# Kernel tuning notes

Hardware: AMD Instinct MI355X
Metric: run time of the kernel (lower is better)

Reference implementation:

```python
import jax, jax.numpy as jnp
import numpy as np
from jax import lax

B, T, D, H = 128, 512, 512, 512
FORGET_BIAS = 1.0  # TF BasicLSTMCell default


def setup_inputs() -> dict:
    key = jax.random.key(0)
    k1, k2, k3 = jax.random.split(key, 3)
    scale = 1.0 / np.sqrt(D + H)
    return {
        "word_vectors": jax.random.normal(k1, (B, T, D), dtype=jnp.float32),
        "num_words": jax.random.randint(k2, (B,), 0, T, dtype=jnp.int32),
        "init_c": jnp.zeros((B, H), dtype=jnp.float32),
        "init_h": jnp.zeros((B, H), dtype=jnp.float32),
        "W": jax.random.normal(k3, (D + H, 4 * H), dtype=jnp.float32) * scale,  # gates i,j,f,o
        "b": jnp.zeros((4 * H,), dtype=jnp.float32),
    }


def reference(word_vectors, num_words, init_c, init_h, W, b):
    # word_vectors: [B, T, D] -> time-major [T, B, D]
    xs = jnp.transpose(word_vectors, (1, 0, 2))
    ts = jnp.arange(T, dtype=num_words.dtype)

    def step(carry, inp):
        c, h = carry
        x, t = inp
        z = jnp.concatenate([x, h], axis=-1) @ W + b  # [B, 4H]
        i, j, f, o = jnp.split(z, 4, axis=-1)  # TF gate order
        new_c = c * jax.nn.sigmoid(f + FORGET_BIAS) + jax.nn.sigmoid(i) * jnp.tanh(j)
        new_h = jnp.tanh(new_c) * jax.nn.sigmoid(o)
        mask = (t < num_words)[:, None]  # [B, 1]
        # static_rnn sequence_length semantics: copy state through, zero outputs
        c2 = jnp.where(mask, new_c, c)
        h2 = jnp.where(mask, new_h, h)
        out = jnp.where(mask, new_h, jnp.zeros_like(new_h))
        return (c2, h2), out

    (final_c, final_h), outputs = lax.scan(step, (init_c, init_h), (xs, ts))
    # outputs: [T, B, H] (time-major, like the list returned by static_rnn)
    return outputs, final_c, final_h
```

## Files before the change

### kernel.cpp

```cpp
#include <hip/hip_runtime.h>


#define B_ 128
#define T_ 512
#define D_ 512
#define H_ 512
#define POLL_CAP 8192

typedef __bf16 bf16x8 __attribute__((ext_vector_type(8)));
typedef float f32x4 __attribute__((ext_vector_type(4)));
typedef unsigned long long u64;

static __device__ __forceinline__ unsigned short f2bf(float f) {
  return __builtin_bit_cast(unsigned short, (__bf16)f);
}
static __device__ __forceinline__ float fast_sigmoid(float x) {
  return __builtin_amdgcn_rcpf(1.f + __expf(-x));
}
static __device__ __forceinline__ float fast_tanh(float x) {
  float xc = fminf(fmaxf(x, -15.f), 15.f);
  float t = __expf(-2.f * xc);
  return (1.f - t) * __builtin_amdgcn_rcpf(1.f + t);
}

#define LBAR()                                             \
  do {                                                     \
    __asm__ volatile("s_waitcnt lgkmcnt(0)" ::: "memory"); \
    __builtin_amdgcn_s_barrier();                          \
    __asm__ volatile("" ::: "memory");                     \
  } while (0)

__global__ __launch_bounds__(256) void pack_w_kernel(const float* __restrict__ W,
                                                     unsigned short* __restrict__ Wp) {
  int tid = blockIdx.x * 256 + threadIdx.x;
  int j = tid & 7;
  int lane = (tid >> 3) & 63;
  int f = tid >> 9;
  int kt = f & 31;
  int w = (f >> 5) & 7;
  int hb = f >> 8;
  int k = (kt << 5) + ((lane >> 4) << 3) + j;
  int cb = lane & 15;
  int col = ((cb >> 2) << 9) + (hb << 5) + (w << 2) + (cb & 3);
  Wp[tid] = f2bf(W[k * 2048 + col]);
}

__global__ __launch_bounds__(1024) void init_ws_kernel(unsigned int* __restrict__ hg) {
  hg[blockIdx.x * 1024 + threadIdx.x] = 0u;
}

__global__ __launch_bounds__(512, 2) void lstm_persistent(
    const float* __restrict__ wv, const int* __restrict__ nw,
    const float* __restrict__ ic, const float* __restrict__ ih,
    const float* __restrict__ bias, const unsigned short* __restrict__ Wp,
    unsigned int* __restrict__ hg, float* __restrict__ out) {
  __shared__ __align__(16) unsigned short hlds[2][16 * 512];
  __shared__ __align__(16) unsigned short xlds[2][16 * 512];

  const int tid = threadIdx.x;
  const int wgid = blockIdx.x;
  const int mg = wgid & 7;
  const int hb = wgid >> 3;
  const int w = tid >> 6;
  const int lane = tid & 63;

  const int q = lane >> 4;
  const int gp = (lane >> 2) & 3;
  const int hc = lane & 3;
  const int er = (q << 2) + gp;
  const int kin = (w << 2) | hc;
  const int grow = (mg << 4) + er;
  const int gcol = (hb << 5) + kin;

  const int nwv = nw[grow];
  float c_reg = ic[grow * H_ + gcol];
  float h_reg = ih[grow * H_ + gcol];

  uint4 wfrag[32];
  {
    const uint4* wp = (const uint4*)Wp + (size_t)((hb * 8 + w) * 32) * 64 + lane;
#pragma unroll
    for (int kt = 0; kt < 32; ++kt) wfrag[kt] = wp[kt * 64];
  }
  const float bv = bias[(gp << 9) + (hb << 5) + kin];

  auto slot64 = [&](int s) { return (u64*)hg + (size_t)(s * 8 + mg) * 4096; };

  const int hslot = (hb << 9) + ((er | ((kin >> 3) << 4)) << 3) + (kin & 7);
  const int ppair = hslot >> 1;

  auto publish_h = [&](u64* dst, unsigned int tag) {
    unsigned int hv = (unsigned int)f2bf(h_reg);
    unsigned int up = (unsigned int)__shfl_down((int)hv, 1);
    if ((lane & 1) == 0) {
      u64 vv = ((u64)tag << 32) | (u64)(hv | (up << 16));
      __hip_atomic_store(dst + ppair, vv, __ATOMIC_RELAXED,
                         __HIP_MEMORY_SCOPE_AGENT);
    }
  };

  auto wait_stage = [&](const u64* s, unsigned int want, unsigned short* dstlds) {
    u64 v0, v1, v2, v3, v4, v5, v6, v7;
    int it = 0;
    while (true) {
      v0 = __hip_atomic_load(s + (((2 * w + 0) << 8) + (0 << 6) + lane), __ATOMIC_RELAXED, __HIP_MEMORY_SCOPE_AGENT);
      v1 = __hip_atomic_load(s + (((2 * w + 0) << 8) + (1 << 6) + lane), __ATOMIC_RELAXED, __HIP_MEMORY_SCOPE_AGENT);
      v2 = __hip_atomic_load(s + (((2 * w + 0) << 8) + (2 << 6) + lane), __ATOMIC_RELAXED, __HIP_MEMORY_SCOPE_AGENT);
      v3 = __hip_atomic_load(s + (((2 * w + 0) << 8) + (3 << 6) + lane), __ATOMIC_RELAXED, __HIP_MEMORY_SCOPE_AGENT);
      v4 = __hip_atomic_load(s + (((2 * w + 1) << 8) + (0 << 6) + lane), __ATOMIC_RELAXED, __HIP_MEMORY_SCOPE_AGENT);
      v5 = __hip_atomic_load(s + (((2 * w + 1) << 8) + (1 << 6) + lane), __ATOMIC_RELAXED, __HIP_MEMORY_SCOPE_AGENT);
      v6 = __hip_atomic_load(s + (((2 * w + 1) << 8) + (2 << 6) + lane), __ATOMIC_RELAXED, __HIP_MEMORY_SCOPE_AGENT);
      v7 = __hip_atomic_load(s + (((2 * w + 1) << 8) + (3 << 6) + lane), __ATOMIC_RELAXED, __HIP_MEMORY_SCOPE_AGENT);
      bool ok = ((unsigned int)(v0 >> 32) == want) && ((unsigned int)(v1 >> 32) == want) &&
                ((unsigned int)(v2 >> 32) == want) && ((unsigned int)(v3 >> 32) == want) &&
                ((unsigned int)(v4 >> 32) == want) && ((unsigned int)(v5 >> 32) == want) &&
                ((unsigned int)(v6 >> 32) == want) && ((unsigned int)(v7 >> 32) == want);
      if (__all(ok)) break;
      if (++it > POLL_CAP) break;
      if (it > 4) __builtin_amdgcn_s_sleep(1);
    }
    unsigned int* d32 = (unsigned int*)dstlds;
    d32[((2 * w + 0) << 8) + (0 << 6) + lane] = (unsigned int)v0;
    d32[((2 * w + 0) << 8) + (1 << 6) + lane] = (unsigned int)v1;
    d32[((2 * w + 0) << 8) + (2 << 6) + lane] = (unsigned int)v2;
    d32[((2 * w + 0) << 8) + (3 << 6) + lane] = (unsigned int)v3;
    d32[((2 * w + 1) << 8) + (0 << 6) + lane] = (unsigned int)v4;
    d32[((2 * w + 1) << 8) + (1 << 6) + lane] = (unsigned int)v5;
    d32[((2 * w + 1) << 8) + (2 << 6) + lane] = (unsigned int)v6;
    d32[((2 * w + 1) << 8) + (3 << 6) + lane] = (unsigned int)v7;
  };

  float4 xr[4];
  auto xissue = [&](int tt) {
    if (tt >= T_) return;
#pragma unroll
    for (int s2 = 0; s2 < 2; ++s2) {
      int e = tid + (s2 << 9);
      int ktx = e >> 6;
      int le = e & 63;
      int r = le & 15;
      int d = (ktx << 5) + ((le >> 4) << 3);
      const float* src = wv + ((size_t)((mg << 4) + r) * T_ + tt) * D_ + d;
      xr[2 * s2] = *(const float4*)src;
      xr[2 * s2 + 1] = *(const float4*)(src + 4);
    }
  };
  auto xcommit = [&](int buf, int tt) {
    if (tt >= T_) return;
#pragma unroll
    for (int s2 = 0; s2 < 2; ++s2) {
      int e = tid + (s2 << 9);
      int ktx = e >> 6;
      int le = e & 63;
      float4 xa = xr[2 * s2], xb = xr[2 * s2 + 1];
      bf16x8 v;
      v[0] = (__bf16)xa.x; v[1] = (__bf16)xa.y; v[2] = (__bf16)xa.z; v[3] = (__bf16)xa.w;
      v[4] = (__bf16)xb.x; v[5] = (__bf16)xb.y; v[6] = (__bf16)xb.z; v[7] = (__bf16)xb.w;
      *(bf16x8*)&xlds[buf][(ktx << 9) + (le << 3)] = v;
    }
  };

  f32x4 xA, xB;
  auto xpart = [&](int buf) {
    f32x4 A = {0.f, 0.f, 0.f, 0.f};
    f32x4 Bc = {0.f, 0.f, 0.f, 0.f};
#pragma unroll
    for (int kt = 0; kt < 8; ++kt) {
      bf16x8 a0 = *(const bf16x8*)&xlds[buf][(kt << 9) + (lane << 3)];
      bf16x8 a1 = *(const bf16x8*)&xlds[buf][((kt + 8) << 9) + (lane << 3)];
      A = __builtin_amdgcn_mfma_f32_16x16x32_bf16(
          a0, __builtin_bit_cast(bf16x8, wfrag[kt]), A, 0, 0, 0);
      Bc = __builtin_amdgcn_mfma_f32_16x16x32_bf16(
          a1, __builtin_bit_cast(bf16x8, wfrag[kt + 8]), Bc, 0, 0, 0);
    }
    xA = A;
    xB = Bc;
  };

  xissue(0); xcommit(0, 0);
  xissue(1); xcommit(1, 1);
#pragma unroll
  for (int s2 = 0; s2 < 2; ++s2) {
    int e = tid + (s2 << 9);
    int ktx = e >> 6;
    int le = e & 63;
    int r = le & 15;
    int d = (ktx << 5) + ((le >> 4) << 3);
    const float* src = ih + (size_t)((mg << 4) + r) * H_ + d;
    float4 ha = *(const float4*)src;
    float4 hbv = *(const float4*)(src + 4);
    bf16x8 v;
    v[0] = (__bf16)ha.x; v[1] = (__bf16)ha.y; v[2] = (__bf16)ha.z; v[3] = (__bf16)ha.w;
    v[4] = (__bf16)hbv.x; v[5] = (__bf16)hbv.y; v[6] = (__bf16)hbv.z; v[7] = (__bf16)hbv.w;
    *(bf16x8*)&hlds[0][(ktx << 9) + (le << 3)] = v;
  }
  __syncthreads();
  xpart(0);

  for (int t = 0; t < T_; ++t) {
    const int par = t & 1;
    u64* hdst = slot64((t + 1) & 1);

    const unsigned short* hsrc = hlds[par];
    f32x4 c0 = xA, c1 = xB;
    f32x4 c2 = {0.f, 0.f, 0.f, 0.f};
    f32x4 c3 = {0.f, 0.f, 0.f, 0.f};
#pragma unroll
    for (int i = 0; i < 4; ++i) {
      bf16x8 a0 = *(const bf16x8*)&hsrc[((4 * i) << 9) + (lane << 3)];
      bf16x8 a1 = *(const bf16x8*)&hsrc[((4 * i + 1) << 9) + (lane << 3)];
      bf16x8 a2 = *(const bf16x8*)&hsrc[((4 * i + 2) << 9) + (lane << 3)];
      bf16x8 a3 = *(const bf16x8*)&hsrc[((4 * i + 3) << 9) + (lane << 3)];
      c0 = __builtin_amdgcn_mfma_f32_16x16x32_bf16(
          a0, __builtin_bit_cast(bf16x8, wfrag[16 + 4 * i]), c0, 0, 0, 0);
      c1 = __builtin_amdgcn_mfma_f32_16x16x32_bf16(
          a1, __builtin_bit_cast(bf16x8, wfrag[17 + 4 * i]), c1, 0, 0, 0);
      c2 = __builtin_amdgcn_mfma_f32_16x16x32_bf16(
          a2, __builtin_bit_cast(bf16x8, wfrag[18 + 4 * i]), c2, 0, 0, 0);
      c3 = __builtin_amdgcn_mfma_f32_16x16x32_bf16(
          a3, __builtin_bit_cast(bf16x8, wfrag[19 + 4 * i]), c3, 0, 0, 0);
    }

    float z0 = (c0[0] + c1[0]) + (c2[0] + c3[0]) + bv;
    float z1 = (c0[1] + c1[1]) + (c2[1] + c3[1]) + bv;
    float z2 = (c0[2] + c1[2]) + (c2[2] + c3[2]) + bv;
    float z3 = (c0[3] + c1[3]) + (c2[3] + c3[3]) + bv;
    {
      bool b0 = gp & 1;
      float e;
      e = __shfl_xor(b0 ? z0 : z1, 4); if (b0) z0 = e; else z1 = e;
      e = __shfl_xor(b0 ? z2 : z3, 4); if (b0) z2 = e; else z3 = e;
      bool b1 = (gp >> 1) & 1;
      e = __shfl_xor(b1 ? z0 : z2, 8); if (b1) z0 = e; else z2 = e;
      e = __shfl_xor(b1 ? z1 : z3, 8); if (b1) z1 = e; else z3 = e;
    }
    {
      float si = fast_sigmoid(z0);
      float tj = fast_tanh(z1);
      float sf = fast_sigmoid(z2 + 1.f);
      float so = fast_sigmoid(z3);
      float nc = c_reg * sf + si * tj;
      float nh = fast_tanh(nc) * so;
      bool m = t < nwv;
      c_reg = m ? nc : c_reg;
      h_reg = m ? nh : h_reg;
      publish_h(hdst, (unsigned int)(t + 1));
      out[(size_t)t * (B_ * H_) + grow * H_ + gcol] = m ? nh : 0.f;
    }

    if (t + 1 < T_) {
      xissue(t + 2);
      xpart(1 - par);
      wait_stage(hdst, (unsigned int)(t + 1), hlds[par ^ 1]);
      xcommit(par, t + 2);
    }
    LBAR();
  }

  size_t base = (size_t)T_ * (B_ * H_);
  out[base + grow * H_ + gcol] = c_reg;
  out[base + B_ * H_ + grow * H_ + gcol] = h_reg;
}

extern "C" void kernel_launch(void* const* d_in, const int* in_sizes, int n_in,
                              void* d_out, int out_size, void* d_ws, size_t ws_size,
                              hipStream_t stream) {
  const float* wv = (const float*)d_in[0];
  const int* nw = (const int*)d_in[1];
  const float* ic = (const float*)d_in[2];
  const float* ih = (const float*)d_in[3];
  const float* W = (const float*)d_in[4];
  const float* bias = (const float*)d_in[5];
  float* out = (float*)d_out;

  char* ws = (char*)d_ws;
  unsigned short* Wp = (unsigned short*)ws;
  unsigned int* hg = (unsigned int*)(ws + (4u << 20));

  init_ws_kernel<<<128, 1024, 0, stream>>>(hg);
  pack_w_kernel<<<(1 << 21) / 256, 256, 0, stream>>>(W, Wp);
  lstm_persistent<<<128, 512, 0, stream>>>(wv, nw, ic, ih, bias, Wp, hg, out);
}
```

Baseline: 1.719 ms.

## Replace tagged h exchange with poison-sentinel slots in an 8-deep ring

The inter-workgroup hidden-state exchange no longer sends a 32-bit step tag alongside each packed bf16 pair. Readiness is now signalled by overwriting a 0xFFFFFFFF poison sentinel, and an 8-slot ring is re-poisoned a few steps ahead. This halves the bytes published and polled per step (4 u64 loads per lane instead of 8). The x prefetch is issued earlier and the output store is moved after the wait to overlap with it. The risk is that a bf16 pair whose bit pattern equals the sentinel (a NaN pair) would stall until the poll cap, and ring reuse relies on the re-poison ordering being correct.

New measurement: 1.848 ms. 1.07x slower.

```diff
diff --git a/kernel.cpp b/kernel.cpp
--- a/kernel.cpp
+++ b/kernel.cpp
@@ -5,6 +5,7 @@
 #define T_ 512
 #define D_ 512
 #define H_ 512
+#define POISON 0xFFFFFFFFu
 #define POLL_CAP 8192
 
 typedef __bf16 bf16x8 __attribute__((ext_vector_type(8)));
@@ -21,6 +22,9 @@
   float xc = fminf(fmaxf(x, -15.f), 15.f);
   float t = __expf(-2.f * xc);
   return (1.f - t) * __builtin_amdgcn_rcpf(1.f + t);
+}
+static __device__ __forceinline__ bool clean64(u64 v) {
+  return ((unsigned int)v != POISON) && ((unsigned int)(v >> 32) != POISON);
 }
 
 #define LBAR()                                             \
@@ -46,7 +50,7 @@
 }
 
 __global__ __launch_bounds__(1024) void init_ws_kernel(unsigned int* __restrict__ hg) {
-  hg[blockIdx.x * 1024 + threadIdx.x] = 0u;
+  hg[blockIdx.x * 1024 + threadIdx.x] = POISON;
 }
 
 __global__ __launch_bounds__(512, 2) void lstm_persistent(
@@ -84,50 +88,46 @@
   }
   const float bv = bias[(gp << 9) + (hb << 5) + kin];
 
-  auto slot64 = [&](int s) { return (u64*)hg + (size_t)(s * 8 + mg) * 4096; };
+  auto slotp = [&](int s) { return hg + (size_t)(s * 8 + mg) * 4096; };
 
   const int hslot = (hb << 9) + ((er | ((kin >> 3) << 4)) << 3) + (kin & 7);
-  const int ppair = hslot >> 1;
-
-  auto publish_h = [&](u64* dst, unsigned int tag) {
+
+  auto publish_h = [&](unsigned int* dst) {
     unsigned int hv = (unsigned int)f2bf(h_reg);
     unsigned int up = (unsigned int)__shfl_down((int)hv, 1);
-    if ((lane & 1) == 0) {
-      u64 vv = ((u64)tag << 32) | (u64)(hv | (up << 16));
-      __hip_atomic_store(dst + ppair, vv, __ATOMIC_RELAXED,
+    if ((lane & 1) == 0)
+      __hip_atomic_store(dst + (hslot >> 1), hv | (up << 16), __ATOMIC_RELAXED,
                          __HIP_MEMORY_SCOPE_AGENT);
-    }
-  };
-
-  auto wait_stage = [&](const u64* s, unsigned int want, unsigned short* dstlds) {
-    u64 v0, v1, v2, v3, v4, v5, v6, v7;
+  };
+
+  auto wait_stage = [&](const unsigned int* slot, unsigned short* dstlds) {
+    const u64* s = (const u64*)slot;
+    const u64* p0 = s + ((2 * w) << 7) + lane;
+    const u64* p1 = p0 + 64;
+    const u64* p2 = s + ((2 * w + 1) << 7) + lane;
+    const u64* p3 = p2 + 64;
+    u64 a0, a1, b0, b1;
     int it = 0;
     while (true) {
-      v0 = __hip_atomic_load(s + (((2 * w + 0) << 8) + (0 << 6) + lane), __ATOMIC_RELAXED, __HIP_MEMORY_SCOPE_AGENT);
-      v1 = __hip_atomic_load(s + (((2 * w + 0) << 8) + (1 << 6) + lane), __ATOMIC_RELAXED, __HIP_MEMORY_SCOPE_AGENT);
-      v2 = __hip_atomic_load(s + (((2 * w + 0) << 8) + (2 << 6) + lane), __ATOMIC_RELAXED, __HIP_MEMORY_SCOPE_AGENT);
-      v3 = __hip_atomic_load(s + (((2 * w + 0) << 8) + (3 << 6) + lane), __ATOMIC_RELAXED, __HIP_MEMORY_SCOPE_AGENT);
-      v4 = __hip_atomic_load(s + (((2 * w + 1) << 8) + (0 << 6) + lane), __ATOMIC_RELAXED, __HIP_MEMORY_SCOPE_AGENT);
-      v5 = __hip_atomic_load(s + (((2 * w + 1) << 8) + (1 << 6) + lane), __ATOMIC_RELAXED, __HIP_MEMORY_SCOPE_AGENT);
-      v6 = __hip_atomic_load(s + (((2 * w + 1) << 8) + (2 << 6) + lane), __ATOMIC_RELAXED, __HIP_MEMORY_SCOPE_AGENT);
-      v7 = __hip_atomic_load(s + (((2 * w + 1) << 8) + (3 << 6) + lane), __ATOMIC_RELAXED, __HIP_MEMORY_SCOPE_AGENT);
-      bool ok = ((unsigned int)(v0 >> 32) == want) && ((unsigned int)(v1 >> 32) == want) &&
-                ((unsigned int)(v2 >> 32) == want) && ((unsigned int)(v3 >> 32) == want) &&
-                ((unsigned int)(v4 >> 32) == want) && ((unsigned int)(v5 >> 32) == want) &&
-                ((unsigned int)(v6 >> 32) == want) && ((unsigned int)(v7 >> 32) == want);
-      if (__all(ok)) break;
+      a0 = __hip_atomic_load(p0, __ATOMIC_RELAXED, __HIP_MEMORY_SCOPE_AGENT);
+      a1 = __hip_atomic_load(p1, __ATOMIC_RELAXED, __HIP_MEMORY_SCOPE_AGENT);
+      b0 = __hip_atomic_load(p2, __ATOMIC_RELAXED, __HIP_MEMORY_SCOPE_AGENT);
+      b1 = __hip_atomic_load(p3, __ATOMIC_RELAXED, __HIP_MEMORY_SCOPE_AGENT);
+      if (__all(clean64(a0) && clean64(a1) && clean64(b0) && clean64(b1))) break;
       if (++it > POLL_CAP) break;
-      if (it > 4) __builtin_amdgcn_s_sleep(1);
-    }
-    unsigned int* d32 = (unsigned int*)dstlds;
-    d32[((2 * w + 0) << 8) + (0 << 6) + lane] = (unsigned int)v0;
-    d32[((2 * w + 0) << 8) + (1 << 6) + lane] = (unsigned int)v1;
-    d32[((2 * w + 0) << 8) + (2 << 6) + lane] = (unsigned int)v2;
-    d32[((2 * w + 0) << 8) + (3 << 6) + lane] = (unsigned int)v3;
-    d32[((2 * w + 1) << 8) + (0 << 6) + lane] = (unsigned int)v4;
-    d32[((2 * w + 1) << 8) + (1 << 6) + lane] = (unsigned int)v5;
-    d32[((2 * w + 1) << 8) + (2 << 6) + lane] = (unsigned int)v6;
-    d32[((2 * w + 1) << 8) + (3 << 6) + lane] = (unsigned int)v7;
+      if (it > 8) __builtin_amdgcn_s_sleep(1);
+    }
+    u64* d = (u64*)dstlds;
+    d[((2 * w) << 7) + lane] = a0;
+    d[((2 * w) << 7) + 64 + lane] = a1;
+    d[((2 * w + 1) << 7) + lane] = b0;
+    d[((2 * w + 1) << 7) + 64 + lane] = b1;
+  };
+
+  auto repoison = [&](unsigned int* slot) {
+    if (tid < 256)
+      __hip_atomic_store(slot + (hb << 8) + tid, POISON, __ATOMIC_RELAXED,
+                         __HIP_MEMORY_SCOPE_AGENT);
   };
 
   float4 xr[4];
@@ -199,7 +199,9 @@
 
   for (int t = 0; t < T_; ++t) {
     const int par = t & 1;
-    u64* hdst = slot64((t + 1) & 1);
+    unsigned int* hdst = slotp((t + 1) & 7);
+
+    xissue(t + 2);
 
     const unsigned short* hsrc = hlds[par];
     f32x4 c0 = xA, c1 = xB;
@@ -234,6 +236,7 @@
       e = __shfl_xor(b1 ? z0 : z2, 8); if (b1) z0 = e; else z2 = e;
       e = __shfl_xor(b1 ? z1 : z3, 8); if (b1) z1 = e; else z3 = e;
     }
+    float outv;
     {
       float si = fast_sigmoid(z0);
       float tj = fast_tanh(z1);
@@ -244,17 +247,20 @@
       bool m = t < nwv;
       c_reg = m ? nc : c_reg;
       h_reg = m ? nh : h_reg;
-      publish_h(hdst, (unsigned int)(t + 1));
-      out[(size_t)t * (B_ * H_) + grow * H_ + gcol] = m ? nh : 0.f;
+      outv = m ? nh : 0.f;
+      if (t + 1 < T_) publish_h(hdst);
     }
 
     if (t + 1 < T_) {
-      xissue(t + 2);
       xpart(1 - par);
-      wait_stage(hdst, (unsigned int)(t + 1), hlds[par ^ 1]);
+      wait_stage(hdst, hlds[par ^ 1]);
+    }
+    out[(size_t)t * (B_ * H_) + grow * H_ + gcol] = outv;
+    if (t + 1 < T_) {
+      repoison(slotp((t + 7) & 7));
       xcommit(par, t + 2);
     }
-    LBAR();
+    if ((t & 3) == 3) __syncthreads(); else LBAR();
   }
 
   size_t base = (size_t)T_ * (B_ * H_);
@@ -277,7 +283,7 @@
   unsigned short* Wp = (unsigned short*)ws;
   unsigned int* hg = (unsigned int*)(ws + (4u << 20));
 
-  init_ws_kernel<<<128, 1024, 0, stream>>>(hg);
+  init_ws_kernel<<<256, 1024, 0, stream>>>(hg);
   pack_w_kernel<<<(1 << 21) / 256, 256, 0, stream>>>(W, Wp);
   lstm_persistent<<<128, 512, 0, stream>>>(wv, nw, ic, ih, bias, Wp, hg, out);
 }
```
